# Optimization experiments

Measured on AMD Instinct MI355X. Metric: run time of the kernel, lower is better.

The kernel has to match this reference:

```python
import jax, jax.numpy as jnp
import numpy as np

N_NODES = 50000
N_EDGES = 800000
D_IN = 128
D_OUT = 128


def setup_inputs() -> dict:
    key = jax.random.key(0)
    k1, k2, k3, k4, k5, k6 = jax.random.split(key, 6)
    x = jax.random.normal(k1, (N_NODES, D_IN), dtype=jnp.float32)
    edge_row = jnp.sort(jax.random.randint(k2, (N_EDGES,), 0, N_NODES, dtype=jnp.int32))
    edge_col = jax.random.randint(k3, (N_EDGES,), 0, N_NODES, dtype=jnp.int32)
    edge_val = jax.random.uniform(k4, (N_EDGES,), dtype=jnp.float32)
    W = jax.random.uniform(k5, (D_OUT, D_IN), dtype=jnp.float32)  # torch Linear weight [out,in], uniform_ init
    b = jax.random.normal(k6, (D_OUT,), dtype=jnp.float32)
    return {"x": x, "edge_row": edge_row, "edge_col": edge_col,
            "edge_val": edge_val, "W": W, "b": b}


def reference(x, edge_row, edge_col, edge_val, W, b):
    # spmm: out[i] = sum_{e: row[e]==i} val[e] * x[col[e]]
    msgs = x[edge_col] * edge_val[:, None]            # [E, D_IN]
    agg = jax.ops.segment_sum(msgs, edge_row, num_segments=x.shape[0])  # [N, D_IN]
    # dropout is identity in eval mode; linear projection y = agg @ W^T + b
    return agg @ W.T + b
```

## Files before the change

### kernel.cpp

```cpp
#include <hip/hip_runtime.h>
#include <hip/hip_bf16.h>


#define NPB     16
#define BLOCK   256
#define D       128
#define CHUNK   512
#define ASTRIDE 136

typedef __attribute__((ext_vector_type(8))) short bf16x8;
typedef __attribute__((ext_vector_type(4))) float f32x4;
typedef __attribute__((ext_vector_type(2))) float v2f;

__device__ __forceinline__ short f2bf(float f) {
    unsigned u = __float_as_uint(f);
    unsigned r = (u + 0x7fffu + ((u >> 16) & 1u)) >> 16;
    return (short)r;
}
__device__ __forceinline__ float bf_lo(int w) { return __int_as_float(w << 16); }
__device__ __forceinline__ float bf_hi(int w) { return __int_as_float(w & 0xffff0000); }

__global__ __launch_bounds__(256)
void prepass_kernel(const float* __restrict__ x,
                    const float* __restrict__ W,
                    const int*   __restrict__ edge_row,
                    short* __restrict__ xb,
                    short* __restrict__ wb,
                    int*   __restrict__ rs,
                    int n_nodes, int n_edges, int n4, int nw4)
{
    const int gid = blockIdx.x * 256 + threadIdx.x;

    if (gid <= n_nodes) {
        int lo = 0, hi = n_edges;
        while (lo < hi) {
            int mid = (lo + hi) >> 1;
            bool lt = (edge_row[mid] < gid);
            lo = lt ? (mid + 1) : lo;
            hi = lt ? hi : mid;
        }
        rs[gid] = lo;
    }

    const int i = gid - (n_nodes + 1);
    if (i >= 0 && i < n4) {
        float4 v = reinterpret_cast<const float4*>(x)[i];
        reinterpret_cast<short4*>(xb)[i] =
            make_short4(f2bf(v.x), f2bf(v.y), f2bf(v.z), f2bf(v.w));
    }

    const int iw = i - n4;
    if (iw >= 0 && iw < nw4) {
        float4 v = reinterpret_cast<const float4*>(W)[iw];
        reinterpret_cast<short4*>(wb)[iw] =
            make_short4(f2bf(v.x), f2bf(v.y), f2bf(v.z), f2bf(v.w));
    }
}

__global__ __launch_bounds__(BLOCK, 6)
void gcn_main_kernel(const short* __restrict__ xb,
                     const short* __restrict__ wb,
                     const int*   __restrict__ rs_g,
                     const int*   __restrict__ edge_col,
                     const float* __restrict__ edge_val,
                     const float* __restrict__ bvec,
                     float*       __restrict__ out,
                     int n_nodes, int n_edges)
{
    __shared__ int2  cv_s[CHUNK];
    __shared__ __align__(16) short agg_s[NPB * ASTRIDE];
    __shared__ int rs_s[NPB + 1];

    const int tid  = threadIdx.x;
    const int wave = tid >> 6;
    const int lane = tid & 63;
    const int tile_base = blockIdx.x * NPB;

    if (tid <= NPB) rs_s[tid] = rs_g[tile_base + tid];
    __syncthreads();

    const int E0 = __builtin_amdgcn_readfirstlane(rs_s[0]);
    const int E1 = __builtin_amdgcn_readfirstlane(rs_s[NPB]);
    const int cnt = min(E1 - E0, CHUNK);

    for (int i = tid; i < cnt; i += BLOCK) {
        cv_s[i] = make_int2(edge_col[E0 + i], __float_as_int(edge_val[E0 + i]));
    }
    __syncthreads();

    const int p = lane >> 4;
    const int q = lane & 15;
    const int n = wave * 4 + p;
    const int e0 = rs_s[n], e1 = rs_s[n + 1];
    const int cap  = E0 + cnt;
    const int ecap = min(e1, cap);
    const short* xq = xb + q * 8;

    v2f acc2[4];
    #pragma unroll
    for (int i = 0; i < 4; ++i) acc2[i] = (v2f){0.f, 0.f};

    for (int e = e0; e < ecap; e += 8) {
        int2  cv[8];
        int4  xr[8];
        #pragma unroll
        for (int u = 0; u < 8; ++u) {
            int idx = e + u;
            int il  = (idx < ecap) ? (idx - E0) : (e0 - E0);
            cv[u] = cv_s[il];
        }
        #pragma unroll
        for (int u = 0; u < 8; ++u) {
            xr[u] = *reinterpret_cast<const int4*>(xq + ((size_t)cv[u].x << 7));
        }
        #pragma unroll
        for (int u = 0; u < 8; ++u) {
            float vm = (e + u < ecap) ? __int_as_float(cv[u].y) : 0.f;
            v2f v2 = (v2f){vm, vm};
            acc2[0] += v2 * (v2f){bf_lo(xr[u].x), bf_hi(xr[u].x)};
            acc2[1] += v2 * (v2f){bf_lo(xr[u].y), bf_hi(xr[u].y)};
            acc2[2] += v2 * (v2f){bf_lo(xr[u].z), bf_hi(xr[u].z)};
            acc2[3] += v2 * (v2f){bf_lo(xr[u].w), bf_hi(xr[u].w)};
        }
    }
    for (int e = max(e0, cap); e < e1; ++e) {
        int   c = edge_col[e];
        float v = edge_val[e];
        int4 xr = *reinterpret_cast<const int4*>(xq + ((size_t)c << 7));
        v2f v2 = (v2f){v, v};
        acc2[0] += v2 * (v2f){bf_lo(xr.x), bf_hi(xr.x)};
        acc2[1] += v2 * (v2f){bf_lo(xr.y), bf_hi(xr.y)};
        acc2[2] += v2 * (v2f){bf_lo(xr.z), bf_hi(xr.z)};
        acc2[3] += v2 * (v2f){bf_lo(xr.w), bf_hi(xr.w)};
    }

    {
        bf16x8 o;
        o[0] = f2bf(acc2[0].x); o[1] = f2bf(acc2[0].y);
        o[2] = f2bf(acc2[1].x); o[3] = f2bf(acc2[1].y);
        o[4] = f2bf(acc2[2].x); o[5] = f2bf(acc2[2].y);
        o[6] = f2bf(acc2[3].x); o[7] = f2bf(acc2[3].y);
        *reinterpret_cast<bf16x8*>(&agg_s[n * ASTRIDE + q * 8]) = o;
    }

    const int n16 = lane & 15;
    const int g   = lane >> 4;

    bf16x8 bfr[2][4];
    float  bj[2];
    #pragma unroll
    for (int tt = 0; tt < 2; ++tt) {
        const int jt = 2 * wave + tt;
        const short* wrow = wb + ((size_t)(jt * 16 + n16)) * D + g * 8;
        #pragma unroll
        for (int ks = 0; ks < 4; ++ks) {
            bfr[tt][ks] = *reinterpret_cast<const bf16x8*>(wrow + ks * 32);
        }
        bj[tt] = bvec[jt * 16 + n16];
    }

    __syncthreads();

    {
        bf16x8 afr[4];
        #pragma unroll
        for (int ks = 0; ks < 4; ++ks) {
            afr[ks] = *reinterpret_cast<const bf16x8*>(
                &agg_s[n16 * ASTRIDE + ks * 32 + g * 8]);
        }

        #pragma unroll
        for (int tt = 0; tt < 2; ++tt) {
            const int jt = 2 * wave + tt;
            const int j  = jt * 16 + n16;

            f32x4 c = {0.f, 0.f, 0.f, 0.f};
            #pragma unroll
            for (int ks = 0; ks < 4; ++ks) {
                c = __builtin_amdgcn_mfma_f32_16x16x32_bf16(afr[ks], bfr[tt][ks], c, 0, 0, 0);
            }
            #pragma unroll
            for (int r = 0; r < 4; ++r) {
                int node = tile_base + g * 4 + r;
                if (node < n_nodes)
                    out[(size_t)node * D + j] = c[r] + bj[tt];
            }
        }
    }
}

__global__ __launch_bounds__(BLOCK, 5)
void gcn_fallback_kernel(const float* __restrict__ x,
                         const int*   __restrict__ edge_row,
                         const int*   __restrict__ edge_col,
                         const float* __restrict__ edge_val,
                         const float* __restrict__ W,
                         const float* __restrict__ bvec,
                         float*       __restrict__ out,
                         int n_nodes, int n_edges)
{
    __shared__ __align__(16) short agg_s[NPB * ASTRIDE];
    __shared__ int rs_s[NPB + 1];

    const int tid  = threadIdx.x;
    const int wave = tid >> 6;
    const int lane = tid & 63;
    const int tile_base = blockIdx.x * NPB;

    if (tid <= NPB) {
        int target = tile_base + tid;
        if (target > n_nodes) target = n_nodes;
        int lo = 0, hi = n_edges;
        while (lo < hi) {
            int mid = (lo + hi) >> 1;
            lo = (edge_row[mid] < target) ? (mid + 1) : lo;
            hi = (edge_row[mid] < target) ? hi : mid;
        }
        rs_s[tid] = lo;
    }
    __syncthreads();

    {
        const int h = lane >> 5;
        const int q = lane & 31;
        const float* xq = x + (q << 2);

        #pragma unroll
        for (int ni = 0; ni < NPB / 4; ++ni) {
            const int n = wave + 4 * ni;
            const int e0 = __builtin_amdgcn_readfirstlane(rs_s[n]);
            const int e1 = __builtin_amdgcn_readfirstlane(rs_s[n + 1]);
            float ax = 0.f, ay = 0.f, az = 0.f, aw = 0.f;
            for (int e = e0; e < e1; e += 16) {
                #pragma unroll
                for (int u = 0; u < 8; ++u) {
                    int idx  = e + 2 * u + h;
                    int idxc = (idx < e1) ? idx : (e1 - 1);
                    int   c  = edge_col[idxc];
                    float vr = edge_val[idxc];
                    float v  = (idx < e1) ? vr : 0.f;
                    float4 xr = *reinterpret_cast<const float4*>(xq + ((size_t)c << 7));
                    ax += v * xr.x; ay += v * xr.y; az += v * xr.z; aw += v * xr.w;
                }
            }
            ax += __shfl_xor(ax, 32, 64); ay += __shfl_xor(ay, 32, 64);
            az += __shfl_xor(az, 32, 64); aw += __shfl_xor(aw, 32, 64);
            if (h == 0) {
                *reinterpret_cast<short4*>(&agg_s[n * ASTRIDE + (q << 2)]) =
                    make_short4(f2bf(ax), f2bf(ay), f2bf(az), f2bf(aw));
            }
        }
    }

    const int n16 = lane & 15;
    const int g   = lane >> 4;
    bf16x8 bfr[2][4];
    #pragma unroll
    for (int tt = 0; tt < 2; ++tt) {
        const int jt = 2 * wave + tt;
        const float* rowp = W + ((size_t)(jt * 16 + n16)) * D + g * 8;
        #pragma unroll
        for (int ks = 0; ks < 4; ++ks) {
            float4 wa  = *reinterpret_cast<const float4*>(rowp + ks * 32);
            float4 wb4 = *reinterpret_cast<const float4*>(rowp + ks * 32 + 4);
            bf16x8 f;
            f[0] = f2bf(wa.x);  f[1] = f2bf(wa.y);  f[2] = f2bf(wa.z);  f[3] = f2bf(wa.w);
            f[4] = f2bf(wb4.x); f[5] = f2bf(wb4.y); f[6] = f2bf(wb4.z); f[7] = f2bf(wb4.w);
            bfr[tt][ks] = f;
        }
    }
    __syncthreads();
    {
        bf16x8 afr[4];
        #pragma unroll
        for (int ks = 0; ks < 4; ++ks)
            afr[ks] = *reinterpret_cast<const bf16x8*>(&agg_s[n16 * ASTRIDE + ks * 32 + g * 8]);
        #pragma unroll
        for (int tt = 0; tt < 2; ++tt) {
            const int jt = 2 * wave + tt;
            const int j  = jt * 16 + n16;
            const float bj = bvec[j];
            f32x4 c = {0.f, 0.f, 0.f, 0.f};
            #pragma unroll
            for (int ks = 0; ks < 4; ++ks)
                c = __builtin_amdgcn_mfma_f32_16x16x32_bf16(afr[ks], bfr[tt][ks], c, 0, 0, 0);
            #pragma unroll
            for (int r = 0; r < 4; ++r) {
                int node = tile_base + g * 4 + r;
                if (node < n_nodes)
                    out[(size_t)node * D + j] = c[r] + bj;
            }
        }
    }
}

extern "C" void kernel_launch(void* const* d_in, const int* in_sizes, int n_in,
                              void* d_out, int out_size, void* d_ws, size_t ws_size,
                              hipStream_t stream) {
    const float* x        = (const float*)d_in[0];
    const int*   edge_row = (const int*)  d_in[1];
    const int*   edge_col = (const int*)  d_in[2];
    const float* edge_val = (const float*)d_in[3];
    const float* W        = (const float*)d_in[4];
    const float* b        = (const float*)d_in[5];
    float* out = (float*)d_out;

    const int n_nodes = in_sizes[0] / D;
    const int n_edges = in_sizes[1];
    const int grid = (n_nodes + NPB - 1) / NPB;

    const size_t xb_bytes = (size_t)n_nodes * D * sizeof(short);
    const size_t rs_bytes = (size_t)(n_nodes + 1) * sizeof(int);
    const size_t wb_bytes = (size_t)D * D * sizeof(short);
    if (ws_size >= xb_bytes + rs_bytes + wb_bytes) {
        short* xb = (short*)d_ws;
        int*   rs = (int*)((char*)d_ws + xb_bytes);
        short* wb = (short*)((char*)d_ws + xb_bytes + rs_bytes);
        const int n4  = n_nodes * D / 4;
        const int nw4 = D * D / 4;
        const int total = (n_nodes + 1) + n4 + nw4;
        prepass_kernel<<<(total + 255) / 256, 256, 0, stream>>>(
            x, W, edge_row, xb, wb, rs, n_nodes, n_edges, n4, nw4);
        gcn_main_kernel<<<grid, BLOCK, 0, stream>>>(xb, wb, rs, edge_col, edge_val,
                                                    b, out, n_nodes, n_edges);
    } else {
        gcn_fallback_kernel<<<grid, BLOCK, 0, stream>>>(x, edge_row, edge_col, edge_val,
                                                        W, b, out, n_nodes, n_edges);
    }
}
```

Measured before the change: 121.9 us.

## Reorder GCN to project features before aggregation, fusing GEMM into prepass

Uses linearity to compute y = x W^T first (MFMA in the prepass, stored as bf16), then aggregates the projected rows in the main kernel and adds bias. This removes the per-tile GEMM, the LDS staging and W loads from the gather kernel, lowers its register and LDS footprint (occupancy hint raised to 7), and drops the separate W conversion. The cost is a bf16 rounding of y before aggregation and a prepass that now does the full dense GEMM over all nodes.

```diff
diff --git a/kernel.cpp b/kernel.cpp
--- a/kernel.cpp
+++ b/kernel.cpp
@@ -20,46 +20,96 @@
 __device__ __forceinline__ float bf_lo(int w) { return __int_as_float(w << 16); }
 __device__ __forceinline__ float bf_hi(int w) { return __int_as_float(w & 0xffff0000); }
 
-__global__ __launch_bounds__(256)
+__global__ __launch_bounds__(256, 4)
 void prepass_kernel(const float* __restrict__ x,
                     const float* __restrict__ W,
                     const int*   __restrict__ edge_row,
-                    short* __restrict__ xb,
-                    short* __restrict__ wb,
+                    short* __restrict__ yb,
                     int*   __restrict__ rs,
-                    int n_nodes, int n_edges, int n4, int nw4)
+                    int n_nodes, int n_edges, int gemm_blocks)
 {
-    const int gid = blockIdx.x * 256 + threadIdx.x;
-
-    if (gid <= n_nodes) {
-        int lo = 0, hi = n_edges;
-        while (lo < hi) {
-            int mid = (lo + hi) >> 1;
-            bool lt = (edge_row[mid] < gid);
-            lo = lt ? (mid + 1) : lo;
-            hi = lt ? hi : mid;
-        }
-        rs[gid] = lo;
-    }
-
-    const int i = gid - (n_nodes + 1);
-    if (i >= 0 && i < n4) {
-        float4 v = reinterpret_cast<const float4*>(x)[i];
-        reinterpret_cast<short4*>(xb)[i] =
+    const int bid = blockIdx.x;
+    const int tid = threadIdx.x;
+
+    if (bid >= gemm_blocks) {
+        const int gid = (bid - gemm_blocks) * 256 + tid;
+        if (gid <= n_nodes) {
+            int lo = 0, hi = n_edges;
+            while (lo < hi) {
+                int mid = (lo + hi) >> 1;
+                bool lt = (edge_row[mid] < gid);
+                lo = lt ? (mid + 1) : lo;
+                hi = lt ? hi : mid;
+            }
+            rs[gid] = lo;
+        }
+        return;
+    }
+
+    __shared__ __align__(16) short xa_s[NPB * ASTRIDE];
+
+    const int wave = tid >> 6;
+    const int lane = tid & 63;
+    const int tile_base = bid * NPB;
+
+    #pragma unroll
+    for (int t = 0; t < 2; ++t) {
+        int idx = tid * 2 + t;
+        int row = idx >> 5;
+        int c4  = idx & 31;
+        int node = tile_base + row;
+        float4 v = (node < n_nodes)
+            ? reinterpret_cast<const float4*>(x)[(size_t)node * 32 + c4]
+            : make_float4(0.f, 0.f, 0.f, 0.f);
+        *reinterpret_cast<short4*>(&xa_s[row * ASTRIDE + c4 * 4]) =
             make_short4(f2bf(v.x), f2bf(v.y), f2bf(v.z), f2bf(v.w));
     }
 
-    const int iw = i - n4;
-    if (iw >= 0 && iw < nw4) {
-        float4 v = reinterpret_cast<const float4*>(W)[iw];
-        reinterpret_cast<short4*>(wb)[iw] =
-            make_short4(f2bf(v.x), f2bf(v.y), f2bf(v.z), f2bf(v.w));
-    }
-}
-
-__global__ __launch_bounds__(BLOCK, 6)
-void gcn_main_kernel(const short* __restrict__ xb,
-                     const short* __restrict__ wb,
+    const int n16 = lane & 15;
+    const int g   = lane >> 4;
+
+    bf16x8 bfr[2][4];
+    #pragma unroll
+    for (int tt = 0; tt < 2; ++tt) {
+        const int jt = 2 * wave + tt;
+        const float* wrow = W + (size_t)(jt * 16 + n16) * D + g * 8;
+        #pragma unroll
+        for (int ks = 0; ks < 4; ++ks) {
+            float4 wa  = *reinterpret_cast<const float4*>(wrow + ks * 32);
+            float4 wb4 = *reinterpret_cast<const float4*>(wrow + ks * 32 + 4);
+            bf16x8 f;
+            f[0] = f2bf(wa.x);  f[1] = f2bf(wa.y);  f[2] = f2bf(wa.z);  f[3] = f2bf(wa.w);
+            f[4] = f2bf(wb4.x); f[5] = f2bf(wb4.y); f[6] = f2bf(wb4.z); f[7] = f2bf(wb4.w);
+            bfr[tt][ks] = f;
+        }
+    }
+
+    __syncthreads();
+
+    bf16x8 afr[4];
+    #pragma unroll
+    for (int ks = 0; ks < 4; ++ks)
+        afr[ks] = *reinterpret_cast<const bf16x8*>(&xa_s[n16 * ASTRIDE + ks * 32 + g * 8]);
+
+    #pragma unroll
+    for (int tt = 0; tt < 2; ++tt) {
+        const int jt = 2 * wave + tt;
+        const int j  = jt * 16 + n16;
+        f32x4 c = {0.f, 0.f, 0.f, 0.f};
+        #pragma unroll
+        for (int ks = 0; ks < 4; ++ks)
+            c = __builtin_amdgcn_mfma_f32_16x16x32_bf16(afr[ks], bfr[tt][ks], c, 0, 0, 0);
+        #pragma unroll
+        for (int r = 0; r < 4; ++r) {
+            int node = tile_base + g * 4 + r;
+            if (node < n_nodes)
+                yb[(size_t)node * D + j] = f2bf(c[r]);
+        }
+    }
+}
+
+__global__ __launch_bounds__(BLOCK, 7)
+void gcn_main_kernel(const short* __restrict__ yb,
                      const int*   __restrict__ rs_g,
                      const int*   __restrict__ edge_col,
                      const float* __restrict__ edge_val,
@@ -67,25 +117,23 @@
                      float*       __restrict__ out,
                      int n_nodes, int n_edges)
 {
-    __shared__ int2  cv_s[CHUNK];
-    __shared__ __align__(16) short agg_s[NPB * ASTRIDE];
-    __shared__ int rs_s[NPB + 1];
+    __shared__ int2 cv_s[CHUNK];
+    __shared__ int  rs_s[NPB + 1];
 
     const int tid  = threadIdx.x;
     const int wave = tid >> 6;
     const int lane = tid & 63;
     const int tile_base = blockIdx.x * NPB;
 
-    if (tid <= NPB) rs_s[tid] = rs_g[tile_base + tid];
+    if (tid <= NPB) rs_s[tid] = rs_g[min(tile_base + tid, n_nodes)];
     __syncthreads();
 
     const int E0 = __builtin_amdgcn_readfirstlane(rs_s[0]);
     const int E1 = __builtin_amdgcn_readfirstlane(rs_s[NPB]);
     const int cnt = min(E1 - E0, CHUNK);
 
-    for (int i = tid; i < cnt; i += BLOCK) {
+    for (int i = tid; i < cnt; i += BLOCK)
         cv_s[i] = make_int2(edge_col[E0 + i], __float_as_int(edge_val[E0 + i]));
-    }
     __syncthreads();
 
     const int p = lane >> 4;
@@ -94,15 +142,15 @@
     const int e0 = rs_s[n], e1 = rs_s[n + 1];
     const int cap  = E0 + cnt;
     const int ecap = min(e1, cap);
-    const short* xq = xb + q * 8;
+    const short* yq = yb + q * 8;
 
     v2f acc2[4];
     #pragma unroll
     for (int i = 0; i < 4; ++i) acc2[i] = (v2f){0.f, 0.f};
 
     for (int e = e0; e < ecap; e += 8) {
-        int2  cv[8];
-        int4  xr[8];
+        int2 cv[8];
+        int4 xr[8];
         #pragma unroll
         for (int u = 0; u < 8; ++u) {
             int idx = e + u;
@@ -110,9 +158,8 @@
             cv[u] = cv_s[il];
         }
         #pragma unroll
-        for (int u = 0; u < 8; ++u) {
-            xr[u] = *reinterpret_cast<const int4*>(xq + ((size_t)cv[u].x << 7));
-        }
+        for (int u = 0; u < 8; ++u)
+            xr[u] = *reinterpret_cast<const int4*>(yq + ((size_t)cv[u].x << 7));
         #pragma unroll
         for (int u = 0; u < 8; ++u) {
             float vm = (e + u < ecap) ? __int_as_float(cv[u].y) : 0.f;
@@ -126,7 +173,7 @@
     for (int e = max(e0, cap); e < e1; ++e) {
         int   c = edge_col[e];
         float v = edge_val[e];
-        int4 xr = *reinterpret_cast<const int4*>(xq + ((size_t)c << 7));
+        int4 xr = *reinterpret_cast<const int4*>(yq + ((size_t)c << 7));
         v2f v2 = (v2f){v, v};
         acc2[0] += v2 * (v2f){bf_lo(xr.x), bf_hi(xr.x)};
         acc2[1] += v2 * (v2f){bf_lo(xr.y), bf_hi(xr.y)};
@@ -134,58 +181,18 @@
         acc2[3] += v2 * (v2f){bf_lo(xr.w), bf_hi(xr.w)};
     }
 
-    {
-        bf16x8 o;
-        o[0] = f2bf(acc2[0].x); o[1] = f2bf(acc2[0].y);
-        o[2] = f2bf(acc2[1].x); o[3] = f2bf(acc2[1].y);
-        o[4] = f2bf(acc2[2].x); o[5] = f2bf(acc2[2].y);
-        o[6] = f2bf(acc2[3].x); o[7] = f2bf(acc2[3].y);
-        *reinterpret_cast<bf16x8*>(&agg_s[n * ASTRIDE + q * 8]) = o;
-    }
-
-    const int n16 = lane & 15;
-    const int g   = lane >> 4;
-
-    bf16x8 bfr[2][4];
-    float  bj[2];
-    #pragma unroll
-    for (int tt = 0; tt < 2; ++tt) {
-        const int jt = 2 * wave + tt;
-        const short* wrow = wb + ((size_t)(jt * 16 + n16)) * D + g * 8;
-        #pragma unroll
-        for (int ks = 0; ks < 4; ++ks) {
-            bfr[tt][ks] = *reinterpret_cast<const bf16x8*>(wrow + ks * 32);
-        }
-        bj[tt] = bvec[jt * 16 + n16];
-    }
-
-    __syncthreads();
-
-    {
-        bf16x8 afr[4];
-        #pragma unroll
-        for (int ks = 0; ks < 4; ++ks) {
-            afr[ks] = *reinterpret_cast<const bf16x8*>(
-                &agg_s[n16 * ASTRIDE + ks * 32 + g * 8]);
-        }
-
-        #pragma unroll
-        for (int tt = 0; tt < 2; ++tt) {
-            const int jt = 2 * wave + tt;
-            const int j  = jt * 16 + n16;
-
-            f32x4 c = {0.f, 0.f, 0.f, 0.f};
-            #pragma unroll
-            for (int ks = 0; ks < 4; ++ks) {
-                c = __builtin_amdgcn_mfma_f32_16x16x32_bf16(afr[ks], bfr[tt][ks], c, 0, 0, 0);
-            }
-            #pragma unroll
-            for (int r = 0; r < 4; ++r) {
-                int node = tile_base + g * 4 + r;
-                if (node < n_nodes)
-                    out[(size_t)node * D + j] = c[r] + bj[tt];
-            }
-        }
+    const int node = tile_base + n;
+    if (node < n_nodes) {
+        const float* bq = bvec + q * 8;
+        float4 b0 = *reinterpret_cast<const float4*>(bq);
+        float4 b1 = *reinterpret_cast<const float4*>(bq + 4);
+        float* orow = out + (size_t)node * D + q * 8;
+        float4 o0 = make_float4(acc2[0].x + b0.x, acc2[0].y + b0.y,
+                                acc2[1].x + b0.z, acc2[1].y + b0.w);
+        float4 o1 = make_float4(acc2[2].x + b1.x, acc2[2].y + b1.y,
+                                acc2[3].x + b1.z, acc2[3].y + b1.w);
+        *reinterpret_cast<float4*>(orow)     = o0;
+        *reinterpret_cast<float4*>(orow + 4) = o1;
     }
 }
 
@@ -309,19 +316,16 @@
     const int n_edges = in_sizes[1];
     const int grid = (n_nodes + NPB - 1) / NPB;
 
-    const size_t xb_bytes = (size_t)n_nodes * D * sizeof(short);
+    const size_t yb_bytes = (size_t)n_nodes * D * sizeof(short);
     const size_t rs_bytes = (size_t)(n_nodes + 1) * sizeof(int);
-    const size_t wb_bytes = (size_t)D * D * sizeof(short);
-    if (ws_size >= xb_bytes + rs_bytes + wb_bytes) {
-        short* xb = (short*)d_ws;
-        int*   rs = (int*)((char*)d_ws + xb_bytes);
-        short* wb = (short*)((char*)d_ws + xb_bytes + rs_bytes);
-        const int n4  = n_nodes * D / 4;
-        const int nw4 = D * D / 4;
-        const int total = (n_nodes + 1) + n4 + nw4;
-        prepass_kernel<<<(total + 255) / 256, 256, 0, stream>>>(
-            x, W, edge_row, xb, wb, rs, n_nodes, n_edges, n4, nw4);
-        gcn_main_kernel<<<grid, BLOCK, 0, stream>>>(xb, wb, rs, edge_col, edge_val,
+    if (ws_size >= yb_bytes + rs_bytes) {
+        short* yb = (short*)d_ws;
+        int*   rs = (int*)((char*)d_ws + yb_bytes);
+        const int gemm_blocks   = grid;
+        const int search_blocks = (n_nodes + 1 + 255) / 256;
+        prepass_kernel<<<gemm_blocks + search_blocks, 256, 0, stream>>>(
+            x, W, edge_row, yb, rs, n_nodes, n_edges, gemm_blocks);
+        gcn_main_kernel<<<grid, BLOCK, 0, stream>>>(yb, rs, edge_col, edge_val,
                                                     b, out, n_nodes, n_edges);
     } else {
         gcn_fallback_kernel<<<grid, BLOCK, 0, stream>>>(x, edge_row, edge_col, edge_val,
```

New measurement: 138.1 us. 13.3% more time.
